# Performance work log

Hardware: AMD Instinct MI355X
Metric: run time of the kernel (lower is better)

Reference implementation:

```python
import jax, jax.numpy as jnp
import numpy as np

B, DIM, T = 8, 512, 4096
INTER = 1536
K = 7
DIL = 1
EPS = 1e-6
LS_INIT = 1e-6


def _ste(x, q):
    # straight-through estimator: forward uses q, gradient flows through x
    return x + jax.lax.stop_gradient(q - x)


def _weight_quant(w):
    # BitNet b1.58 ternary weight quant with per-tensor scale = mean(|w|)
    s = jnp.clip(jnp.mean(jnp.abs(w)), 1e-5, None)
    q = jnp.clip(jnp.round(w / s), -1.0, 1.0) * s
    return _ste(w, q)


def _act_quant(x, axis):
    # per-token int8 absmax quant along `axis`
    s = 127.0 / jnp.clip(jnp.max(jnp.abs(x), axis=axis, keepdims=True), 1e-5, None)
    q = jnp.clip(jnp.round(x * s), -128.0, 127.0) / s
    return _ste(x, q)


def setup_inputs() -> dict:
    key = jax.random.key(0)
    ks = jax.random.split(key, 5)
    return {
        "x": jax.random.normal(ks[0], (B, DIM, T), dtype=jnp.float32),
        "dw_w": jax.random.normal(ks[1], (DIM, 1, K), dtype=jnp.float32) * 0.1,
        "dw_b": jnp.zeros((DIM,), jnp.float32),
        "ln_g": jnp.ones((DIM,), jnp.float32),
        "ln_b": jnp.zeros((DIM,), jnp.float32),
        "w1": jax.random.normal(ks[2], (INTER, DIM), dtype=jnp.float32) * (1.0 / np.sqrt(DIM)),
        "b1": jnp.zeros((INTER,), jnp.float32),
        "w2": jax.random.normal(ks[3], (DIM, INTER), dtype=jnp.float32) * (1.0 / np.sqrt(INTER)),
        "b2": jnp.zeros((DIM,), jnp.float32),
        "gamma": LS_INIT * jnp.ones((DIM,), jnp.float32),
    }


def reference(x, dw_w, dw_b, ln_g, ln_b, w1, b1, w2, b2, gamma):
    residual = x  # [B, DIM, T]
    pad = (K + (DIL - 1) * (K - 1)) // 2
    # quantized depthwise conv1d
    xq = _act_quant(x, axis=1)
    wq = _weight_quant(dw_w)  # [DIM, 1, K]
    y = jax.lax.conv_general_dilated(
        xq, wq, window_strides=(1,), padding=[(pad, pad)],
        rhs_dilation=(DIL,), dimension_numbers=("NCH", "OIH", "NCH"),
        feature_group_count=DIM,
    ) + dw_b[None, :, None]
    y = y.transpose(0, 2, 1)  # [B, T, DIM]
    # LayerNorm over channels
    mu = jnp.mean(y, axis=-1, keepdims=True)
    var = jnp.var(y, axis=-1, keepdims=True)
    y = (y - mu) * jax.lax.rsqrt(var + EPS) * ln_g + ln_b
    # BitLinear 1 -> GELU -> BitLinear 2
    h = jnp.einsum("btc,fc->btf", _act_quant(y, -1), _weight_quant(w1)) + b1
    h = jax.nn.gelu(h, approximate=False)
    o = jnp.einsum("btf,cf->btc", _act_quant(h, -1), _weight_quant(w2)) + b2
    o = gamma * o
    return residual + o.transpose(0, 2, 1)  # [B, DIM, T]
```

## Files before the change

### kernel.cpp

```cpp
#include <hip/hip_runtime.h>
#include <hip/hip_bf16.h>

#define BATCH 8
#define DIM   512
#define TLEN  4096
#define INTER 1536
#define NTOK  (BATCH*TLEN)

#define QH 15.875f
#define DH (1.0f/15.875f)

typedef __attribute__((ext_vector_type(4))) float f32x4;
typedef __attribute__((ext_vector_type(8))) short s16x8;
typedef __attribute__((ext_vector_type(4))) int   i32x4;
typedef signed char i8;

__device__ __forceinline__ float bf2f(short s) {
  unsigned u = ((unsigned)(unsigned short)s) << 16;
  return __uint_as_float(u);
}
__device__ __forceinline__ short f2bf(float f) {
  union { __hip_bfloat16 h; unsigned short u; } cv;
  cv.h = __float2bfloat16(f);
  return (short)cv.u;
}
__device__ __forceinline__ void async16(void* lds, const void* g) {
  __builtin_amdgcn_global_load_lds((const __attribute__((address_space(1))) void*)g,
                                   (__attribute__((address_space(3))) void*)lds, 16, 0, 0);
}
__device__ __forceinline__ float gelu_sig(float h) {
  float e = __builtin_amdgcn_exp2f(-2.4554669f * h);
  return h * __builtin_amdgcn_rcpf(1.f + e);
}

#define VMW(N) asm volatile("s_waitcnt vmcnt(" #N ")" ::: "memory")
#define LKW0() asm volatile("s_waitcnt lgkmcnt(0)" ::: "memory")

__global__ __launch_bounds__(256)
void reduce_abs3_k(const float* __restrict__ w1, const float* __restrict__ w2,
                   const float* __restrict__ dww, float* __restrict__ ws) {
  const int b = blockIdx.x, tid = threadIdx.x;
  const float* w; int n, nb, lb; float* part;
  if (b < 128)      { w = w1;  n = INTER * DIM; nb = 128; lb = b;       part = ws + 16; }
  else if (b < 256) { w = w2;  n = INTER * DIM; nb = 128; lb = b - 128; part = ws + 144; }
  else              { w = dww; n = DIM * 7;     nb = 8;   lb = b - 256; part = ws + 272; }
  float s = 0.f;
  for (int i = lb * 256 + tid; i < n; i += nb * 256) s += fabsf(w[i]);
  #pragma unroll
  for (int off = 32; off; off >>= 1) s += __shfl_xor(s, off);
  __shared__ float ls[4];
  if ((tid & 63) == 0) ls[tid >> 6] = s;
  __syncthreads();
  if (tid == 0) part[lb] = ls[0] + ls[1] + ls[2] + ls[3];
}

__global__ void finalize_scales_k(float* __restrict__ ws) {
  const int tid = threadIdx.x;
  const int seg = tid >> 6, lane = tid & 63;
  float s;
  if (seg == 0)      s = ws[16 + lane] + ws[16 + 64 + lane];
  else if (seg == 1) s = ws[144 + lane] + ws[144 + 64 + lane];
  else               s = (lane < 8) ? ws[272 + lane] : 0.f;
  #pragma unroll
  for (int off = 32; off; off >>= 1) s += __shfl_xor(s, off);
  if (lane == 0) {
    if (seg == 0)      ws[0] = fmaxf(s / 786432.f, 1e-5f);
    else if (seg == 1) ws[1] = fmaxf(s / 786432.f, 1e-5f);
    else               ws[2] = fmaxf(s / 3584.f, 1e-5f);
  }
}

__global__ __launch_bounds__(256)
void quant_w8_both_k(const float* __restrict__ w1, const float* __restrict__ w2,
                     const float* __restrict__ sc,
                     i8* __restrict__ w1q, i8* __restrict__ w2q) {
  const int bid = blockIdx.x;
  if (bid < 3072) {
    int i = bid * 256 + threadIdx.x;
    w1q[i] = (i8)(int)fminf(fmaxf(rintf(w1[i] / sc[0]), -1.f), 1.f);
  } else {
    int i = (bid - 3072) * 256 + threadIdx.x;
    w2q[i] = (i8)(int)fminf(fmaxf(rintf(w2[i] / sc[1]), -1.f), 1.f);
  }
}

__global__ __launch_bounds__(512)
void conv_ln_quant_k(const float* __restrict__ x, const float* __restrict__ dww,
                     const float* __restrict__ dwb, const float* __restrict__ lng,
                     const float* __restrict__ lnb,
                     const float* __restrict__ scales, i8* __restrict__ yq,
                     float* __restrict__ siy) {
  __shared__ short axs[512 * 44];
  __shared__ short ly[32 * 512];
  __shared__ float sx[40], sxi[40];
  const int tid = threadIdx.x;
  const int b = blockIdx.y;
  const int t0 = blockIdx.x * 32;
  const int lane = tid & 63, w = tid >> 6;

  const bool interior = (t0 >= 4) && (t0 + 36 <= TLEN);
  #pragma unroll 2
  for (int p = 0; p < 10; ++p) {
    const int g = p * 512 + tid;
    const int c = g / 10;
    const int ch = g - c * 10;
    const float* xr = x + ((size_t)b * DIM + c) * TLEN + (t0 - 4) + ch * 4;
    f32x4 L;
    if (interior) {
      L = *(const f32x4*)xr;
    } else {
      #pragma unroll
      for (int e = 0; e < 4; ++e) {
        int tg = t0 - 4 + ch * 4 + e;
        L[e] = (tg >= 0 && tg < TLEN) ? xr[e] : 0.f;
      }
    }
    uint2 pk;
    pk.x = (unsigned)(unsigned short)f2bf(L[0]) |
           ((unsigned)(unsigned short)f2bf(L[1]) << 16);
    pk.y = (unsigned)(unsigned short)f2bf(L[2]) |
           ((unsigned)(unsigned short)f2bf(L[3]) << 16);
    *(uint2*)((char*)axs + c * 88 + ch * 8) = pk;
  }
  __syncthreads();

  if (w < 5) {
    const int j = w * 8 + (lane & 7);
    const int cg = lane >> 3;
    float m = 0.f;
    #pragma unroll 4
    for (int cc = 0; cc < 64; ++cc)
      m = fmaxf(m, fabsf(bf2f(axs[(cg + 8 * cc) * 44 + j])));
    m = fmaxf(m, __shfl_xor(m, 8));
    m = fmaxf(m, __shfl_xor(m, 16));
    m = fmaxf(m, __shfl_xor(m, 32));
    if (cg == 0) {
      int tg = t0 - 4 + j;
      float a = (tg >= 0 && tg < TLEN) ? fmaxf(m, 1e-5f) : 1.f;
      sx[j] = 127.f / a;
      sxi[j] = a * (1.f / 127.f);
    }
  }
  __syncthreads();

  {
    const float sdw = scales[2];
    const float rs = 1.f / sdw;
    const int c = tid;
    float wv[7];
    #pragma unroll
    for (int k = 0; k < 7; ++k)
      wv[k] = fminf(fmaxf(rintf(dww[c * 7 + k] * rs), -1.f), 1.f) * sdw;
    const float bias = dwb[c];
    const char* xr = (const char*)axs + c * 88;

    #define UNPKQ(u, Q) do {                                                \
      const uint2 v_ = *(const uint2*)(xr + 8 * (u));                       \
      float r_[4];                                                          \
      r_[0] = bf2f((short)(v_.x & 0xffff));                                 \
      r_[1] = bf2f((short)(v_.x >> 16));                                    \
      r_[2] = bf2f((short)(v_.y & 0xffff));                                 \
      r_[3] = bf2f((short)(v_.y >> 16));                                    \
      _Pragma("unroll")                                                     \
      for (int e_ = 0; e_ < 4; ++e_) {                                      \
        const int j_ = 4 * (u) + e_;                                        \
        Q[e_] = fminf(fmaxf(rintf(r_[e_] * sx[j_]), -128.f), 127.f) * sxi[j_]; \
      }                                                                     \
    } while (0)

    f32x4 A0, A1, A2;
    UNPKQ(0, A0); UNPKQ(1, A1);
    #pragma unroll 1
    for (int u = 0; u < 8; ++u) {
      UNPKQ(u + 2, A2);
      #pragma unroll
      for (int s = 0; s < 4; ++s) {
        float a0 = bias;
        #pragma unroll
        for (int k = 0; k < 7; ++k) {
          const int i = s + 1 + k;
          const float qa = (i < 4) ? A0[i & 3] : (i < 8) ? A1[i & 3] : A2[i & 3];
          a0 += wv[k] * qa;
        }
        const int t = 4 * u + s;
        *(short*)((char*)ly + t * 1024 + c * 2) = f2bf(a0);
      }
      A0 = A1; A1 = A2;
    }
    #undef UNPKQ
  }
  __syncthreads();

  float gg[8], bb[8];
  #pragma unroll
  for (int j = 0; j < 8; ++j) { gg[j] = lng[lane * 8 + j]; bb[j] = lnb[lane * 8 + j]; }
  #pragma unroll 1
  for (int i = 0; i < 4; ++i) {
    const int t = w * 4 + i;
    s16x8 v = *(const s16x8*)((char*)ly + t * 1024 + lane * 16);
    float f[8];
    float s = 0.f, sq = 0.f;
    #pragma unroll
    for (int j = 0; j < 8; ++j) { f[j] = bf2f(v[j]); s += f[j]; sq += f[j] * f[j]; }
    #pragma unroll
    for (int off = 32; off; off >>= 1) { s += __shfl_xor(s, off); sq += __shfl_xor(sq, off); }
    const float mu = s * (1.f / 512.f);
    const float var = sq * (1.f / 512.f) - mu * mu;
    const float rstd = rsqrtf(var + 1e-6f);
    float amx = 0.f;
    #pragma unroll
    for (int j = 0; j < 8; ++j) {
      f[j] = (f[j] - mu) * rstd * gg[j] + bb[j];
      amx = fmaxf(amx, fabsf(f[j]));
    }
    #pragma unroll
    for (int off = 32; off; off >>= 1) amx = fmaxf(amx, __shfl_xor(amx, off));
    const float m = fmaxf(amx, 1e-5f);
    const float ss = 127.f / m;
    const int tok = b * TLEN + t0 + t;
    if (lane == 0) siy[tok] = m * (1.f / 127.f);
    unsigned lo = 0, hi = 0;
    #pragma unroll
    for (int j = 0; j < 4; ++j) {
      int q = (int)fminf(fmaxf(rintf(f[j] * ss), -128.f), 127.f);
      lo |= ((unsigned)(q & 255)) << (8 * j);
    }
    #pragma unroll
    for (int j = 4; j < 8; ++j) {
      int q = (int)fminf(fmaxf(rintf(f[j] * ss), -128.f), 127.f);
      hi |= ((unsigned)(q & 255)) << (8 * (j - 4));
    }
    uint2 pk; pk.x = lo; pk.y = hi;
    const int tl = t & 7;
    const int ch = (lane >> 1) ^ tl;
    *(uint2*)(yq + (size_t)tok * DIM + ch * 16 + (lane & 1) * 8) = pk;
  }
}

__global__ __launch_bounds__(512, 2)
void fused_ffn_k(const i8* __restrict__ yq, const i8* __restrict__ w1q,
                 const i8* __restrict__ w2q, const float* __restrict__ b1,
                 const float* __restrict__ b2, const float* __restrict__ gamma,
                 const float* __restrict__ siy, const float* __restrict__ scales,
                 const float* __restrict__ x, float* __restrict__ out) {
  __shared__ i8 smem[163840];
  i8* const yql = smem;
  i8* const hql = smem + 65536;
  const int tid = threadIdx.x;
  const int t0 = blockIdx.x * 64;
  const int lane = tid & 63, w = tid >> 6;
  const int lc = lane & 15, lg = lane >> 4;
  const int srow = lane >> 2, schk = lane & 3;
  i8* const myst = smem + 32768 + w * 4096;

  #pragma unroll
  for (int l = 0; l < 4; ++l)
    async16(yql + l * 8192 + tid * 16, yq + (size_t)t0 * DIM + l * 8192 + tid * 16);

  #define STAGE1(s) do {                                                      \
    const int ftp_ = (s) >> 3, kt_ = (s) & 7;                                 \
    _Pragma("unroll")                                                         \
    for (int q_ = 0; q_ < 4; ++q_) {                                          \
      const int rr_ = q_ * 16 + srow;                                         \
      const int sc_ = schk ^ ((rr_ >> 1) & 3);                                \
      async16(myst + q_ * 1024 + lane * 16,                                   \
              w1q + (size_t)(ftp_ * 512 + w * 64 + rr_) * DIM + kt_ * 64 + sc_ * 16); \
    }                                                                         \
  } while (0)

  STAGE1(0);
  asm volatile("" ::: "memory");
  VMW(4);
  __builtin_amdgcn_s_barrier();

  const float sw1 = scales[0];
  float sy[4];
  #pragma unroll
  for (int j = 0; j < 4; ++j) sy[j] = siy[t0 + j * 16 + lc] * sw1;

  i32x4 acc[4][4] = {};
  for (int ftp = 0; ftp < 3; ++ftp) {
    #pragma unroll
    for (int kt = 0; kt < 8; ++kt) {
      const int s = ftp * 8 + kt;
      VMW(0);
      i32x4 af[4], bf[4];
      #pragma unroll
      for (int i_ = 0; i_ < 4; ++i_) {
        const int ar = i_ * 16 + lc;
        af[i_] = *(const i32x4*)(myst + ar * 64 + ((lg ^ ((ar >> 1) & 3)) << 4));
      }
      #pragma unroll
      for (int j_ = 0; j_ < 4; ++j_) {
        const int tok = j_ * 16 + lc;
        bf[j_] = *(const i32x4*)(yql + tok * 512 + (((kt * 4 + lg) ^ (tok & 7)) << 4));
      }
      LKW0();
      __builtin_amdgcn_sched_barrier(0);
      if (s + 1 < 24) STAGE1(s + 1);
      __builtin_amdgcn_s_setprio(1);
      #pragma unroll
      for (int i_ = 0; i_ < 4; ++i_)
        #pragma unroll
        for (int j_ = 0; j_ < 4; ++j_)
          acc[i_][j_] = __builtin_amdgcn_mfma_i32_16x16x64_i8(af[i_], bf[j_],
                                                              acc[i_][j_], 0, 0, 0);
      __builtin_amdgcn_s_setprio(0);
      if (kt == 7) {
        #pragma unroll
        for (int i_ = 0; i_ < 4; ++i_) {
          const int f0_ = ftp * 512 + w * 64 + i_ * 16 + lg * 4;
          const int cb_ = ftp * 32 + w * 4 + i_;
          float b1v_[4];
          #pragma unroll
          for (int r_ = 0; r_ < 4; ++r_) b1v_[r_] = b1[f0_ + r_];
          #pragma unroll
          for (int j_ = 0; j_ < 4; ++j_) {
            const int tok_ = j_ * 16 + lc;
            unsigned pk_ = 0;
            #pragma unroll
            for (int r_ = 0; r_ < 4; ++r_) {
              float hv_ = fmaf((float)acc[i_][j_][r_], sy[j_], b1v_[r_]);
              float gv_ = gelu_sig(hv_);
              int q_ = (int)rintf(__builtin_amdgcn_fmed3f(gv_ * QH, -128.f, 127.f));
              pk_ |= ((unsigned)(q_ & 255)) << (8 * r_);
              acc[i_][j_][r_] = 0;
            }
            *(unsigned*)(hql + tok_ * 1536 + (((cb_ ^ (tok_ & 7)) << 4) + lg * 4)) = pk_;
          }
        }
      }
    }
  }
  #undef STAGE1
  __syncthreads();

  #define STAGE2(s) do {                                                      \
    _Pragma("unroll")                                                         \
    for (int q_ = 0; q_ < 4; ++q_) {                                          \
      const int rr_ = q_ * 16 + srow;                                         \
      const int sc_ = schk ^ ((rr_ >> 1) & 3);                                \
      async16(myst + q_ * 1024 + lane * 16,                                   \
              w2q + (size_t)(w * 64 + rr_) * INTER + (s) * 64 + sc_ * 16);    \
    }                                                                         \
  } while (0)

  STAGE2(0);
  i32x4 a3[4][4] = {};
  #pragma unroll 4
  for (int s = 0; s < 24; ++s) {
    VMW(0);
    i32x4 af[4], bf[4];
    #pragma unroll
    for (int i_ = 0; i_ < 4; ++i_) {
      const int ar = i_ * 16 + lc;
      af[i_] = *(const i32x4*)(myst + ar * 64 + ((lg ^ ((ar >> 1) & 3)) << 4));
    }
    #pragma unroll
    for (int j_ = 0; j_ < 4; ++j_) {
      const int tok = j_ * 16 + lc;
      bf[j_] = *(const i32x4*)(hql + tok * 1536 + (((s * 4 + lg) ^ (tok & 7)) << 4));
    }
    LKW0();
    __builtin_amdgcn_sched_barrier(0);
    if (s + 1 < 24) STAGE2(s + 1);
    __builtin_amdgcn_s_setprio(1);
    #pragma unroll
    for (int i_ = 0; i_ < 4; ++i_)
      #pragma unroll
      for (int j_ = 0; j_ < 4; ++j_)
        a3[i_][j_] = __builtin_amdgcn_mfma_i32_16x16x64_i8(af[i_], bf[j_],
                                                           a3[i_][j_], 0, 0, 0);
    __builtin_amdgcn_s_setprio(0);
  }
  #undef STAGE2

  const float dq = scales[1] * DH;
  #pragma unroll
  for (int i = 0; i < 4; ++i) {
    const int c0 = w * 64 + i * 16 + lg * 4;
    #pragma unroll
    for (int j = 0; j < 4; ++j) {
      const int tok = t0 + j * 16 + lc;
      const int bb = tok >> 12;
      const int tt = tok & 4095;
      #pragma unroll
      for (int r = 0; r < 4; ++r) {
        const int c = c0 + r;
        float o = (float)a3[i][j][r] * dq + b2[c];
        size_t idx = ((size_t)(bb * DIM + c)) * TLEN + tt;
        out[idx] = x[idx] + gamma[c] * o;
      }
    }
  }
}

extern "C" void kernel_launch(void* const* d_in, const int* in_sizes, int n_in,
                              void* d_out, int out_size, void* d_ws, size_t ws_size,
                              hipStream_t stream) {
  const float* x    = (const float*)d_in[0];
  const float* dww  = (const float*)d_in[1];
  const float* dwb  = (const float*)d_in[2];
  const float* lng  = (const float*)d_in[3];
  const float* lnb  = (const float*)d_in[4];
  const float* w1   = (const float*)d_in[5];
  const float* b1   = (const float*)d_in[6];
  const float* w2   = (const float*)d_in[7];
  const float* b2   = (const float*)d_in[8];
  const float* gam  = (const float*)d_in[9];
  float* out = (float*)d_out;

  const size_t NEEDED = 18616320;
  if (ws_size < NEEDED) return;

  char* ws = (char*)d_ws;
  float* scales = (float*)ws;
  float* siy    = (float*)(ws + 135168);
  i8* w1q       = (i8*)(ws + 266240);
  i8* w2q       = (i8*)(ws + 1052672);
  i8* yq        = (i8*)(ws + 1839104);

  reduce_abs3_k<<<264, 256, 0, stream>>>(w1, w2, dww, scales);
  finalize_scales_k<<<1, 192, 0, stream>>>(scales);
  quant_w8_both_k<<<6144, 256, 0, stream>>>(w1, w2, scales, w1q, w2q);
  conv_ln_quant_k<<<dim3(TLEN / 32, BATCH), 512, 0, stream>>>(x, dww, dwb, lng, lnb,
                                                              scales, yq, siy);
  fused_ffn_k<<<NTOK / 64, 512, 0, stream>>>(yq, w1q, w2q, b1, b2, gam, siy,
                                             scales, x, out);
}
```

Measured before the change: 159.8 us.

## Halve token tile to 32 per block to raise FFN kernel occupancy

Shrinks the fused FFN block from 64 to 32 tokens, halving LDS usage and per-wave register tiles, and raises launch bounds to allow more resident blocks. Stage 1 now iterates over six feature chunks and stage 2 splits output channels into two passes with prefetch across the pass boundary. This trades per-weight data reuse (each weight tile now feeds half the MFMAs, doubling weight traffic) for more concurrent waves and better latency hiding.

```diff
diff --git a/kernel.cpp b/kernel.cpp
--- a/kernel.cpp
+++ b/kernel.cpp
@@ -237,162 +237,163 @@
   }
 }
 
-__global__ __launch_bounds__(512, 2)
+__global__ __launch_bounds__(512, 4)
 void fused_ffn_k(const i8* __restrict__ yq, const i8* __restrict__ w1q,
                  const i8* __restrict__ w2q, const float* __restrict__ b1,
                  const float* __restrict__ b2, const float* __restrict__ gamma,
                  const float* __restrict__ siy, const float* __restrict__ scales,
                  const float* __restrict__ x, float* __restrict__ out) {
-  __shared__ i8 smem[163840];
+  __shared__ i8 smem[81920];
   i8* const yql = smem;
-  i8* const hql = smem + 65536;
+  i8* const hql = smem + 32768;
   const int tid = threadIdx.x;
-  const int t0 = blockIdx.x * 64;
+  const int t0 = blockIdx.x * 32;
   const int lane = tid & 63, w = tid >> 6;
   const int lc = lane & 15, lg = lane >> 4;
   const int srow = lane >> 2, schk = lane & 3;
-  i8* const myst = smem + 32768 + w * 4096;
-
-  #pragma unroll
-  for (int l = 0; l < 4; ++l)
-    async16(yql + l * 8192 + tid * 16, yq + (size_t)t0 * DIM + l * 8192 + tid * 16);
+  i8* const myst = smem + 16384 + w * 2048;
+
+  async16(yql + tid * 16, yq + (size_t)t0 * DIM + tid * 16);
+  async16(yql + 8192 + tid * 16, yq + (size_t)t0 * DIM + 8192 + tid * 16);
 
   #define STAGE1(s) do {                                                      \
     const int ftp_ = (s) >> 3, kt_ = (s) & 7;                                 \
     _Pragma("unroll")                                                         \
-    for (int q_ = 0; q_ < 4; ++q_) {                                          \
+    for (int q_ = 0; q_ < 2; ++q_) {                                          \
       const int rr_ = q_ * 16 + srow;                                         \
       const int sc_ = schk ^ ((rr_ >> 1) & 3);                                \
       async16(myst + q_ * 1024 + lane * 16,                                   \
-              w1q + (size_t)(ftp_ * 512 + w * 64 + rr_) * DIM + kt_ * 64 + sc_ * 16); \
+              w1q + (size_t)(ftp_ * 256 + w * 32 + rr_) * DIM + kt_ * 64 + sc_ * 16); \
     }                                                                         \
   } while (0)
 
   STAGE1(0);
   asm volatile("" ::: "memory");
-  VMW(4);
+  VMW(2);
   __builtin_amdgcn_s_barrier();
 
   const float sw1 = scales[0];
-  float sy[4];
+  float sy[2];
   #pragma unroll
-  for (int j = 0; j < 4; ++j) sy[j] = siy[t0 + j * 16 + lc] * sw1;
-
-  i32x4 acc[4][4] = {};
-  for (int ftp = 0; ftp < 3; ++ftp) {
+  for (int j = 0; j < 2; ++j) sy[j] = siy[t0 + j * 16 + lc] * sw1;
+
+  i32x4 acc[2][2] = {};
+  #pragma unroll 1
+  for (int ftp = 0; ftp < 6; ++ftp) {
     #pragma unroll
     for (int kt = 0; kt < 8; ++kt) {
       const int s = ftp * 8 + kt;
       VMW(0);
-      i32x4 af[4], bf[4];
-      #pragma unroll
-      for (int i_ = 0; i_ < 4; ++i_) {
+      i32x4 af[2], bf[2];
+      #pragma unroll
+      for (int i_ = 0; i_ < 2; ++i_) {
         const int ar = i_ * 16 + lc;
         af[i_] = *(const i32x4*)(myst + ar * 64 + ((lg ^ ((ar >> 1) & 3)) << 4));
       }
       #pragma unroll
-      for (int j_ = 0; j_ < 4; ++j_) {
+      for (int j_ = 0; j_ < 2; ++j_) {
         const int tok = j_ * 16 + lc;
         bf[j_] = *(const i32x4*)(yql + tok * 512 + (((kt * 4 + lg) ^ (tok & 7)) << 4));
       }
       LKW0();
       __builtin_amdgcn_sched_barrier(0);
-      if (s + 1 < 24) STAGE1(s + 1);
+      if (s + 1 < 48) STAGE1(s + 1);
       __builtin_amdgcn_s_setprio(1);
       #pragma unroll
-      for (int i_ = 0; i_ < 4; ++i_)
+      for (int i_ = 0; i_ < 2; ++i_)
         #pragma unroll
-        for (int j_ = 0; j_ < 4; ++j_)
+        for (int j_ = 0; j_ < 2; ++j_)
           acc[i_][j_] = __builtin_amdgcn_mfma_i32_16x16x64_i8(af[i_], bf[j_],
                                                               acc[i_][j_], 0, 0, 0);
       __builtin_amdgcn_s_setprio(0);
-      if (kt == 7) {
+    }
+    #pragma unroll
+    for (int i_ = 0; i_ < 2; ++i_) {
+      const int f0_ = ftp * 256 + w * 32 + i_ * 16 + lg * 4;
+      const int cb_ = ftp * 16 + w * 2 + i_;
+      float b1v_[4];
+      #pragma unroll
+      for (int r_ = 0; r_ < 4; ++r_) b1v_[r_] = b1[f0_ + r_];
+      #pragma unroll
+      for (int j_ = 0; j_ < 2; ++j_) {
+        const int tok_ = j_ * 16 + lc;
+        unsigned pk_ = 0;
         #pragma unroll
-        for (int i_ = 0; i_ < 4; ++i_) {
-          const int f0_ = ftp * 512 + w * 64 + i_ * 16 + lg * 4;
-          const int cb_ = ftp * 32 + w * 4 + i_;
-          float b1v_[4];
-          #pragma unroll
-          for (int r_ = 0; r_ < 4; ++r_) b1v_[r_] = b1[f0_ + r_];
-          #pragma unroll
-          for (int j_ = 0; j_ < 4; ++j_) {
-            const int tok_ = j_ * 16 + lc;
-            unsigned pk_ = 0;
-            #pragma unroll
-            for (int r_ = 0; r_ < 4; ++r_) {
-              float hv_ = fmaf((float)acc[i_][j_][r_], sy[j_], b1v_[r_]);
-              float gv_ = gelu_sig(hv_);
-              int q_ = (int)rintf(__builtin_amdgcn_fmed3f(gv_ * QH, -128.f, 127.f));
-              pk_ |= ((unsigned)(q_ & 255)) << (8 * r_);
-              acc[i_][j_][r_] = 0;
-            }
-            *(unsigned*)(hql + tok_ * 1536 + (((cb_ ^ (tok_ & 7)) << 4) + lg * 4)) = pk_;
-          }
+        for (int r_ = 0; r_ < 4; ++r_) {
+          float hv_ = fmaf((float)acc[i_][j_][r_], sy[j_], b1v_[r_]);
+          float gv_ = gelu_sig(hv_);
+          int q_ = (int)rintf(__builtin_amdgcn_fmed3f(gv_ * QH, -128.f, 127.f));
+          pk_ |= ((unsigned)(q_ & 255)) << (8 * r_);
+          acc[i_][j_][r_] = 0;
         }
+        *(unsigned*)(hql + tok_ * 1536 + (((cb_ ^ (tok_ & 7)) << 4) + lg * 4)) = pk_;
       }
     }
   }
   #undef STAGE1
   __syncthreads();
 
-  #define STAGE2(s) do {                                                      \
+  #define STAGE2(cp, s) do {                                                  \
     _Pragma("unroll")                                                         \
-    for (int q_ = 0; q_ < 4; ++q_) {                                          \
+    for (int q_ = 0; q_ < 2; ++q_) {                                          \
       const int rr_ = q_ * 16 + srow;                                         \
       const int sc_ = schk ^ ((rr_ >> 1) & 3);                                \
       async16(myst + q_ * 1024 + lane * 16,                                   \
-              w2q + (size_t)(w * 64 + rr_) * INTER + (s) * 64 + sc_ * 16);    \
+              w2q + (size_t)((cp) * 256 + w * 32 + rr_) * INTER + (s) * 64 + sc_ * 16); \
     }                                                                         \
   } while (0)
 
-  STAGE2(0);
-  i32x4 a3[4][4] = {};
-  #pragma unroll 4
-  for (int s = 0; s < 24; ++s) {
-    VMW(0);
-    i32x4 af[4], bf[4];
-    #pragma unroll
-    for (int i_ = 0; i_ < 4; ++i_) {
-      const int ar = i_ * 16 + lc;
-      af[i_] = *(const i32x4*)(myst + ar * 64 + ((lg ^ ((ar >> 1) & 3)) << 4));
-    }
-    #pragma unroll
-    for (int j_ = 0; j_ < 4; ++j_) {
-      const int tok = j_ * 16 + lc;
-      bf[j_] = *(const i32x4*)(hql + tok * 1536 + (((s * 4 + lg) ^ (tok & 7)) << 4));
-    }
-    LKW0();
-    __builtin_amdgcn_sched_barrier(0);
-    if (s + 1 < 24) STAGE2(s + 1);
-    __builtin_amdgcn_s_setprio(1);
-    #pragma unroll
-    for (int i_ = 0; i_ < 4; ++i_)
-      #pragma unroll
-      for (int j_ = 0; j_ < 4; ++j_)
-        a3[i_][j_] = __builtin_amdgcn_mfma_i32_16x16x64_i8(af[i_], bf[j_],
-                                                           a3[i_][j_], 0, 0, 0);
-    __builtin_amdgcn_s_setprio(0);
+  const float dq = scales[1] * DH;
+  const int bb = t0 >> 12;
+  const int tt0 = t0 & 4095;
+  #pragma unroll 1
+  for (int cp = 0; cp < 2; ++cp) {
+    STAGE2(cp, 0);
+    i32x4 a3[2][2] = {};
+    #pragma unroll
+    for (int s = 0; s < 24; ++s) {
+      VMW(0);
+      i32x4 af[2], bf[2];
+      #pragma unroll
+      for (int i_ = 0; i_ < 2; ++i_) {
+        const int ar = i_ * 16 + lc;
+        af[i_] = *(const i32x4*)(myst + ar * 64 + ((lg ^ ((ar >> 1) & 3)) << 4));
+      }
+      #pragma unroll
+      for (int j_ = 0; j_ < 2; ++j_) {
+        const int tok = j_ * 16 + lc;
+        bf[j_] = *(const i32x4*)(hql + tok * 1536 + (((s * 4 + lg) ^ (tok & 7)) << 4));
+      }
+      LKW0();
+      __builtin_amdgcn_sched_barrier(0);
+      if (s + 1 < 24) STAGE2(cp, s + 1);
+      else if (cp == 0) STAGE2(1, 0);
+      __builtin_amdgcn_s_setprio(1);
+      #pragma unroll
+      for (int i_ = 0; i_ < 2; ++i_)
+        #pragma unroll
+        for (int j_ = 0; j_ < 2; ++j_)
+          a3[i_][j_] = __builtin_amdgcn_mfma_i32_16x16x64_i8(af[i_], bf[j_],
+                                                             a3[i_][j_], 0, 0, 0);
+      __builtin_amdgcn_s_setprio(0);
+    }
+    #pragma unroll
+    for (int i_ = 0; i_ < 2; ++i_) {
+      const int c0 = cp * 256 + w * 32 + i_ * 16 + lg * 4;
+      #pragma unroll
+      for (int j_ = 0; j_ < 2; ++j_) {
+        const int tt = tt0 + j_ * 16 + lc;
+        #pragma unroll
+        for (int r_ = 0; r_ < 4; ++r_) {
+          const int c = c0 + r_;
+          float o = (float)a3[i_][j_][r_] * dq + b2[c];
+          size_t idx = ((size_t)(bb * DIM + c)) * TLEN + tt;
+          out[idx] = x[idx] + gamma[c] * o;
+        }
+      }
+    }
   }
   #undef STAGE2
-
-  const float dq = scales[1] * DH;
-  #pragma unroll
-  for (int i = 0; i < 4; ++i) {
-    const int c0 = w * 64 + i * 16 + lg * 4;
-    #pragma unroll
-    for (int j = 0; j < 4; ++j) {
-      const int tok = t0 + j * 16 + lc;
-      const int bb = tok >> 12;
-      const int tt = tok & 4095;
-      #pragma unroll
-      for (int r = 0; r < 4; ++r) {
-        const int c = c0 + r;
-        float o = (float)a3[i][j][r] * dq + b2[c];
-        size_t idx = ((size_t)(bb * DIM + c)) * TLEN + tt;
-        out[idx] = x[idx] + gamma[c] * o;
-      }
-    }
-  }
 }
 
 extern "C" void kernel_launch(void* const* d_in, const int* in_sizes, int n_in,
@@ -425,6 +426,6 @@
   quant_w8_both_k<<<6144, 256, 0, stream>>>(w1, w2, scales, w1q, w2q);
   conv_ln_quant_k<<<dim3(TLEN / 32, BATCH), 512, 0, stream>>>(x, dww, dwb, lng, lnb,
                                                               scales, yq, siy);
-  fused_ffn_k<<<NTOK / 64, 512, 0, stream>>>(yq, w1q, w2q, b1, b2, gam, siy,
+  fused_ffn_k<<<NTOK / 32, 512, 0, stream>>>(yq, w1q, w2q, b1, b2, gam, siy,
                                              scales, x, out);
 }
```

Result: slower. 194.6 us (+21.7%).
